# Optimization experiments

Hardware: AMD Instinct MI355X
Metric: run time of the kernel (lower is better)

The kernel has to match this reference:

```python
import jax, jax.numpy as jnp
import numpy as np

NEG_SLOPE = 0.2
EPS = 1e-16


def _gat_layer(x, src, dst, W, a_src, a_dst, b, n_nodes):
    # x: [N, Fin], W: [Fout, Fin]; src/dst: [E'] (self-loops already appended)
    h = x @ W.T                              # [N, Fout]
    alpha_s = h @ a_src                      # [N] per-source score
    alpha_d = h @ a_dst                      # [N] per-dest score
    e = jax.nn.leaky_relu(alpha_s[src] + alpha_d[dst], NEG_SLOPE)  # [E']
    # segment softmax over destination nodes (PyG softmax semantics)
    m = jax.ops.segment_max(e, dst, num_segments=n_nodes)          # [N]
    ex = jnp.exp(e - m[dst])                                       # [E']
    s = jax.ops.segment_sum(ex, dst, num_segments=n_nodes)         # [N]
    alpha = ex / (s[dst] + EPS)                                    # [E']
    out = jax.ops.segment_sum(alpha[:, None] * h[src], dst, num_segments=n_nodes)
    return out + b, alpha


def setup_inputs() -> dict:
    key = jax.random.key(0)
    ks = jax.random.split(key, 14)
    N, E, F_IN, H1, H2, F_OUT = 50000, 800000, 128, 64, 64, 32
    sc = 0.1
    return {
        "x": jax.random.normal(ks[0], (N, F_IN), dtype=jnp.float32),
        "edge_index": jax.random.randint(ks[1], (2, E), 0, N, dtype=jnp.int64),
        "W1": jax.random.normal(ks[2], (H1, F_IN), dtype=jnp.float32) * sc,
        "a_src1": jax.random.normal(ks[3], (H1,), dtype=jnp.float32) * sc,
        "a_dst1": jax.random.normal(ks[4], (H1,), dtype=jnp.float32) * sc,
        "b1": jnp.zeros((H1,), dtype=jnp.float32),
        "W2": jax.random.normal(ks[5], (H2, H1), dtype=jnp.float32) * sc,
        "a_src2": jax.random.normal(ks[6], (H2,), dtype=jnp.float32) * sc,
        "a_dst2": jax.random.normal(ks[7], (H2,), dtype=jnp.float32) * sc,
        "b2": jnp.zeros((H2,), dtype=jnp.float32),
        "W3": jax.random.normal(ks[8], (F_OUT, H2), dtype=jnp.float32) * sc,
        "a_src3": jax.random.normal(ks[9], (F_OUT,), dtype=jnp.float32) * sc,
        "a_dst3": jax.random.normal(ks[10], (F_OUT,), dtype=jnp.float32) * sc,
        "b3": jnp.zeros((F_OUT,), dtype=jnp.float32),
    }


def reference(x, edge_index, W1, a_src1, a_dst1, b1, W2, a_src2, a_dst2, b2, W3, a_src3, a_dst3, b3):
    N = x.shape[0]
    loops = jnp.arange(N, dtype=edge_index.dtype)
    src = jnp.concatenate([edge_index[0], loops])  # add_self_loops=True
    dst = jnp.concatenate([edge_index[1], loops])

    h, alpha1 = _gat_layer(x, src, dst, W1, a_src1, a_dst1, b1, N)
    h = jax.nn.relu(h)
    h, _ = _gat_layer(h, src, dst, W2, a_src2, a_dst2, b2, N)
    h = jax.nn.relu(h)
    out, _ = _gat_layer(h, src, dst, W3, a_src3, a_dst3, b3, N)
    # att_tuple = (edge_index with self loops, attention coefficients of layer 1)
    return (jnp.stack([src, dst]), alpha1, out)
```

## Files before the change

kernel.cpp:

```cpp
#include <hip/hip_runtime.h>
#include <hip/hip_bf16.h>
#include <math.h>

#define NEG_SLOPE 0.2f
#define GAT_EPS 1e-16f

constexpr int NN = 50000;
constexpr int NE = 800000;
constexpr int EP = NE + NN;
constexpr int NB = (NN + 255) / 256;

constexpr int PB  = 128;
constexpr int PT  = 1024;
constexpr int CH  = (EP + PB - 1) / PB;
constexpr int NCH = 4;
constexpr int BPC = PB / NCH;

__device__ inline void edge_sd(const int* __restrict__ ei, int i, int& s, int& d) {
    if (i < NE) { s = ei[i]; d = ei[NE + i]; }
    else        { s = d = i - NE; }
}

__device__ inline float bflo(unsigned int h) { return __uint_as_float(h << 16); }
__device__ inline float bfhi(unsigned int h) { return __uint_as_float(h & 0xffff0000u); }

__global__ __launch_bounds__(PT) void k_p1_hist(const int* __restrict__ ei,
                                                float* __restrict__ out0,
                                                unsigned char* __restrict__ hist,
                                                unsigned char* __restrict__ rank8) {
    __shared__ unsigned int sh[NN / 4];
    int b = blockIdx.x, t = threadIdx.x;
    for (int w = t; w < NN / 4; w += PT) sh[w] = 0u;
    __syncthreads();
    int i0 = b * CH;
    int iend = i0 + CH; if (iend > EP) iend = EP;
    for (int i = i0 + t; i < iend; i += PT) {
        int s, d; edge_sd(ei, i, s, d);
        __builtin_nontemporal_store((float)s, &out0[i]);
        __builtin_nontemporal_store((float)d, &out0[EP + i]);
        int sft = (d & 3) * 8;
        unsigned int old = atomicAdd(&sh[d >> 2], 1u << sft);
        __builtin_nontemporal_store((unsigned char)(old >> sft), &rank8[i]);
    }
    __syncthreads();
    unsigned int* hw = (unsigned int*)(hist + (size_t)b * NN);
    for (int w = t; w < NN / 4; w += PT) hw[w] = sh[w];
}

__global__ __launch_bounds__(256) void k_p2_scan(unsigned char* __restrict__ hist,
                                                 unsigned char* __restrict__ chunksum) {
    int n = blockIdx.x * 256 + threadIdx.x;
    int c = blockIdx.y;
    if (n >= NN) return;
    unsigned int run = 0;
    size_t idx = (size_t)(c * BPC) * NN + n;
    for (int b = 0; b < BPC; ++b, idx += NN) {
        unsigned int v = hist[idx];
        hist[idx] = (unsigned char)run;
        run += v;
    }
    chunksum[n * NCH + c] = (unsigned char)run;
}

__global__ void k_scan1(const unsigned char* __restrict__ chunksum,
                        unsigned char* __restrict__ chunkoff,
                        int* __restrict__ rowptr, int* __restrict__ bsum) {
    __shared__ int sh[256];
    int t = threadIdx.x, i = blockIdx.x * 256 + t;
    int v = 0;
    if (i < NN) {
        unsigned int cs = *(const unsigned int*)&chunksum[i * 4];
        unsigned int c0 = cs & 0xffu, c1 = (cs >> 8) & 0xffu;
        unsigned int c2 = (cs >> 16) & 0xffu, c3 = cs >> 24;
        unsigned int o1 = c0, o2 = c0 + c1, o3 = c0 + c1 + c2;
        *(unsigned int*)&chunkoff[i * 4] = (o1 << 8) | (o2 << 16) | (o3 << 24);
        v = (int)(o3 + c3);
    }
    sh[t] = v; __syncthreads();
    for (int off = 1; off < 256; off <<= 1) {
        int x = (t >= off) ? sh[t - off] : 0;
        __syncthreads();
        sh[t] += x;
        __syncthreads();
    }
    if (i < NN) rowptr[i] = sh[t] - v;
    if (t == 255) bsum[blockIdx.x] = sh[255];
}

__global__ void k_scan2(int* __restrict__ bsum, int* __restrict__ boff) {
    __shared__ int sh[256];
    int t = threadIdx.x;
    int v = (t < NB) ? bsum[t] : 0;
    sh[t] = v; __syncthreads();
    for (int off = 1; off < 256; off <<= 1) {
        int x = (t >= off) ? sh[t - off] : 0;
        __syncthreads();
        sh[t] += x;
        __syncthreads();
    }
    if (t < NB) boff[t] = sh[t] - v;
}

__global__ void k_scan3(int* __restrict__ rowptr, const int* __restrict__ boff) {
    int i = blockIdx.x * blockDim.x + threadIdx.x;
    if (i < NN) rowptr[i] += boff[i >> 8];
    if (i == 0) rowptr[NN] = EP;
}

__global__ __launch_bounds__(PT) void k_fill(const int* __restrict__ ei,
                                             const unsigned char* __restrict__ rank8,
                                             const unsigned char* __restrict__ hist,
                                             const unsigned char* __restrict__ chunkoff,
                                             const int* __restrict__ rowptr,
                                             unsigned short* __restrict__ col) {
    int b = blockIdx.x, t = threadIdx.x;
    int c = b / BPC;
    const unsigned char* __restrict__ hrow = hist + (size_t)b * NN;
    int i0 = b * CH;
    int iend = i0 + CH; if (iend > EP) iend = EP;
    for (int i = i0 + t; i < iend; i += PT) {
        int s, d; edge_sd(ei, i, s, d);
        int pos = rowptr[d] + (int)chunkoff[d * 4 + c] + (int)hrow[d] + (int)rank8[i];
        col[pos] = (unsigned short)s;
    }
}

__global__ void k_alpha_out(const int* __restrict__ ei, const float* __restrict__ as_,
                            const float* __restrict__ ad_, const float* __restrict__ inv,
                            float* __restrict__ out_alpha) {
    int i = blockIdx.x * blockDim.x + threadIdx.x;
    if (i >= EP) return;
    int s, d; edge_sd(ei, i, s, d);
    float v = as_[s] + ad_[d];
    v = v > 0.f ? v : NEG_SLOPE * v;
    __builtin_nontemporal_store(__expf(v) * inv[d], &out_alpha[i]);
}

struct alignas(8) bh4 { __hip_bfloat16 a, b, c, d; };

__device__ inline void fma4(float4& acc, float x, const float4& w) {
    acc.x = fmaf(x, w.x, acc.x);
    acc.y = fmaf(x, w.y, acc.y);
    acc.z = fmaf(x, w.z, acc.z);
    acc.w = fmaf(x, w.w, acc.w);
}

template <int FIN, int FOUT, int NPB>
__global__ __launch_bounds__(256) void k_gemm_t(const float* __restrict__ in,
                                                const float* __restrict__ W,
                                                const float* __restrict__ avs,
                                                const float* __restrict__ avd,
                                                __hip_bfloat16* __restrict__ H,
                                                float* __restrict__ as_,
                                                float* __restrict__ ad_, int n) {
    constexpr int TF = FOUT / 4;
    constexpr int XS = FIN + 4;
    constexpr int WS = FOUT + 4;
    __shared__ float sX[NPB * XS];
    __shared__ float sWt[FIN * WS];
    int tid = threadIdx.x;
    for (int idx = tid; idx < FIN * FOUT; idx += 256) {
        int f = idx % FOUT, k = idx / FOUT;
        sWt[k * WS + f] = W[f * FIN + k];
    }
    int nb = blockIdx.x * NPB;
    for (int idx = tid; idx < NPB * (FIN / 4); idx += 256) {
        int node = idx / (FIN / 4), kq = idx % (FIN / 4);
        int g = nb + node;
        float4 v = make_float4(0.f, 0.f, 0.f, 0.f);
        if (g < n) v = *(const float4*)&in[(size_t)g * FIN + kq * 4];
        *(float4*)&sX[node * XS + kq * 4] = v;
    }
    __syncthreads();

    int fq = tid % TF, ng = tid / TF;
    int n0 = ng * 4;
    float4 acc0 = make_float4(0.f, 0.f, 0.f, 0.f);
    float4 acc1 = acc0, acc2 = acc0, acc3 = acc0;
    for (int k = 0; k < FIN; k += 4) {
        float4 w0 = *(const float4*)&sWt[(k + 0) * WS + fq * 4];
        float4 w1 = *(const float4*)&sWt[(k + 1) * WS + fq * 4];
        float4 w2 = *(const float4*)&sWt[(k + 2) * WS + fq * 4];
        float4 w3 = *(const float4*)&sWt[(k + 3) * WS + fq * 4];
        float4 x0 = *(const float4*)&sX[(n0 + 0) * XS + k];
        float4 x1 = *(const float4*)&sX[(n0 + 1) * XS + k];
        float4 x2 = *(const float4*)&sX[(n0 + 2) * XS + k];
        float4 x3 = *(const float4*)&sX[(n0 + 3) * XS + k];
        fma4(acc0, x0.x, w0); fma4(acc0, x0.y, w1); fma4(acc0, x0.z, w2); fma4(acc0, x0.w, w3);
        fma4(acc1, x1.x, w0); fma4(acc1, x1.y, w1); fma4(acc1, x1.z, w2); fma4(acc1, x1.w, w3);
        fma4(acc2, x2.x, w0); fma4(acc2, x2.y, w1); fma4(acc2, x2.z, w2); fma4(acc2, x2.w, w3);
        fma4(acc3, x3.x, w0); fma4(acc3, x3.y, w1); fma4(acc3, x3.z, w2); fma4(acc3, x3.w, w3);
    }
    float4 accs[4] = {acc0, acc1, acc2, acc3};
    float4 vs4 = *(const float4*)&avs[fq * 4];
    float4 vd4 = *(const float4*)&avd[fq * 4];
#pragma unroll
    for (int j = 0; j < 4; ++j) {
        int g = nb + n0 + j;
        float ps = accs[j].x * vs4.x + accs[j].y * vs4.y + accs[j].z * vs4.z + accs[j].w * vs4.w;
        float pd = accs[j].x * vd4.x + accs[j].y * vd4.y + accs[j].z * vd4.z + accs[j].w * vd4.w;
#pragma unroll
        for (int off = TF / 2; off; off >>= 1) {
            ps += __shfl_down(ps, off, TF);
            pd += __shfl_down(pd, off, TF);
        }
        if (g < n) {
            if (fq == 0) { as_[g] = ps; ad_[g] = pd; }
            bh4 o;
            o.a = __float2bfloat16(accs[j].x);
            o.b = __float2bfloat16(accs[j].y);
            o.c = __float2bfloat16(accs[j].z);
            o.d = __float2bfloat16(accs[j].w);
            *(bh4*)&H[(size_t)g * FOUT + fq * 4] = o;
        }
    }
}

template <int FOUT, bool RELU, bool WRITE_INV>
__global__ __launch_bounds__(256) void k_node_attn(
    const int* __restrict__ rowptr, const unsigned short* __restrict__ col,
    const float* __restrict__ as_, const float* __restrict__ ad_,
    const __hip_bfloat16* __restrict__ H, const float* __restrict__ bias,
    float* __restrict__ outp, float* __restrict__ inv_out) {
    int wid = (blockIdx.x * blockDim.x + threadIdx.x) >> 6;
    int lane = threadIdx.x & 63;
    if (wid >= NN) return;
    int start = rowptr[wid], end = rowptr[wid + 1];
    float adv = ad_[wid];
    const uint2* __restrict__ H4 = (const uint2*)H;

    float sloc = 0.f;
    float ax = 0.f, ay = 0.f, az = 0.f, aw = 0.f;
    for (int c = start; c < end; c += 64) {
        int e = c + lane;
        float p = 0.f;
        int sc = 0;
        if (e < end) {
            sc = (int)col[e];
            float v = as_[sc] + adv;
            v = v > 0.f ? v : NEG_SLOPE * v;
            p = __expf(v);
        }
        sloc += p;
        int cnt = end - c; if (cnt > 64) cnt = 64;
        if (FOUT == 64) {
            int q = lane >> 4, fl = lane & 15;
            int j = 0;
            for (; j + 32 <= cnt; j += 32) {
                float pp[8]; int ss[8]; uint2 hh[8];
#pragma unroll
                for (int k = 0; k < 8; ++k) {
                    int ek = j + 4 * k + q;
                    pp[k] = __shfl(p, ek);
                    ss[k] = __shfl(sc, ek);
                }
#pragma unroll
                for (int k = 0; k < 8; ++k) hh[k] = H4[((size_t)ss[k] << 4) + fl];
#pragma unroll
                for (int k = 0; k < 8; ++k) {
                    ax = fmaf(pp[k], bflo(hh[k].x), ax);
                    ay = fmaf(pp[k], bfhi(hh[k].x), ay);
                    az = fmaf(pp[k], bflo(hh[k].y), az);
                    aw = fmaf(pp[k], bfhi(hh[k].y), aw);
                }
            }
            for (; j + 8 <= cnt; j += 8) {
                int e0 = j + q, e1 = j + 4 + q;
                float p0 = __shfl(p, e0), p1 = __shfl(p, e1);
                int s0 = __shfl(sc, e0), s1 = __shfl(sc, e1);
                uint2 h0 = H4[((size_t)s0 << 4) + fl];
                uint2 h1 = H4[((size_t)s1 << 4) + fl];
                ax = fmaf(p0, bflo(h0.x), ax); ay = fmaf(p0, bfhi(h0.x), ay);
                az = fmaf(p0, bflo(h0.y), az); aw = fmaf(p0, bfhi(h0.y), aw);
                ax = fmaf(p1, bflo(h1.x), ax); ay = fmaf(p1, bfhi(h1.x), ay);
                az = fmaf(p1, bflo(h1.y), az); aw = fmaf(p1, bfhi(h1.y), aw);
            }
            for (; j < cnt; j += 4) {
                int e0 = j + q;
                float p0 = __shfl(p, e0);
                int   s0 = __shfl(sc, e0);
                uint2 h0 = H4[((size_t)s0 << 4) + fl];
                ax = fmaf(p0, bflo(h0.x), ax); ay = fmaf(p0, bfhi(h0.x), ay);
                az = fmaf(p0, bflo(h0.y), az); aw = fmaf(p0, bfhi(h0.y), aw);
            }
        } else {
            int oc = lane >> 3, fl = lane & 7;
            int j = 0;
            for (; j + 32 <= cnt; j += 32) {
                float pp[4]; int ss[4]; uint2 hh[4];
#pragma unroll
                for (int k = 0; k < 4; ++k) {
                    int ek = j + 8 * k + oc;
                    pp[k] = __shfl(p, ek);
                    ss[k] = __shfl(sc, ek);
                }
#pragma unroll
                for (int k = 0; k < 4; ++k) hh[k] = H4[((size_t)ss[k] << 3) + fl];
#pragma unroll
                for (int k = 0; k < 4; ++k) {
                    ax = fmaf(pp[k], bflo(hh[k].x), ax);
                    ay = fmaf(pp[k], bfhi(hh[k].x), ay);
                    az = fmaf(pp[k], bflo(hh[k].y), az);
                    aw = fmaf(pp[k], bfhi(hh[k].y), aw);
                }
            }
            for (; j < cnt; j += 8) {
                int e0 = j + oc;
                float p0 = __shfl(p, e0);
                int   s0 = __shfl(sc, e0);
                uint2 h0 = H4[((size_t)s0 << 3) + fl];
                ax = fmaf(p0, bflo(h0.x), ax); ay = fmaf(p0, bfhi(h0.x), ay);
                az = fmaf(p0, bflo(h0.y), az); aw = fmaf(p0, bfhi(h0.y), aw);
            }
        }
    }
    for (int off = 32; off; off >>= 1) sloc += __shfl_xor(sloc, off);
    float inv = 1.f / (sloc + GAT_EPS);
    if (WRITE_INV && lane == 0) inv_out[wid] = inv;

    if (FOUT == 64) {
        ax += __shfl_xor(ax, 16); ay += __shfl_xor(ay, 16);
        az += __shfl_xor(az, 16); aw += __shfl_xor(aw, 16);
        ax += __shfl_xor(ax, 32); ay += __shfl_xor(ay, 32);
        az += __shfl_xor(az, 32); aw += __shfl_xor(aw, 32);
        if (lane < 16) {
            float4 bb = *(const float4*)&bias[lane * 4];
            float o0 = bb.x + ax * inv;
            float o1 = bb.y + ay * inv;
            float o2 = bb.z + az * inv;
            float o3 = bb.w + aw * inv;
            if (RELU) {
                o0 = fmaxf(o0, 0.f); o1 = fmaxf(o1, 0.f);
                o2 = fmaxf(o2, 0.f); o3 = fmaxf(o3, 0.f);
            }
            *(float4*)&outp[((size_t)wid << 6) + lane * 4] = make_float4(o0, o1, o2, o3);
        }
    } else {
        ax += __shfl_xor(ax, 8);  ay += __shfl_xor(ay, 8);
        az += __shfl_xor(az, 8);  aw += __shfl_xor(aw, 8);
        ax += __shfl_xor(ax, 16); ay += __shfl_xor(ay, 16);
        az += __shfl_xor(az, 16); aw += __shfl_xor(aw, 16);
        ax += __shfl_xor(ax, 32); ay += __shfl_xor(ay, 32);
        az += __shfl_xor(az, 32); aw += __shfl_xor(aw, 32);
        if (lane < 8) {
            float4 bb = *(const float4*)&bias[lane * 4];
            float o0 = bb.x + ax * inv;
            float o1 = bb.y + ay * inv;
            float o2 = bb.z + az * inv;
            float o3 = bb.w + aw * inv;
            if (RELU) {
                o0 = fmaxf(o0, 0.f); o1 = fmaxf(o1, 0.f);
                o2 = fmaxf(o2, 0.f); o3 = fmaxf(o3, 0.f);
            }
            *(float4*)&outp[((size_t)wid << 5) + lane * 4] = make_float4(o0, o1, o2, o3);
        }
    }
}

extern "C" void kernel_launch(void* const* d_in, const int* in_sizes, int n_in,
                              void* d_out, int out_size, void* d_ws, size_t ws_size,
                              hipStream_t stream) {
    const float* x  = (const float*)d_in[0];
    const int*   ei = (const int*)d_in[1];
    const float* W1 = (const float*)d_in[2];
    const float* as1 = (const float*)d_in[3];
    const float* ad1 = (const float*)d_in[4];
    const float* b1 = (const float*)d_in[5];
    const float* W2 = (const float*)d_in[6];
    const float* as2 = (const float*)d_in[7];
    const float* ad2 = (const float*)d_in[8];
    const float* b2 = (const float*)d_in[9];
    const float* W3 = (const float*)d_in[10];
    const float* as3 = (const float*)d_in[11];
    const float* ad3 = (const float*)d_in[12];
    const float* b3 = (const float*)d_in[13];

    float* out = (float*)d_out;
    float* out_edges = out;
    float* out_alpha = out + 2 * EP;
    float* out_final = out + 3 * EP;

    char* w = (char*)d_ws;
    size_t o = 0;
    auto alloc = [&](size_t bytes) { void* p = w + o; o = (o + bytes + 15) & ~15ull; return p; };
    float* as_ = (float*)alloc((size_t)NN * 4);
    float* ad_ = (float*)alloc((size_t)NN * 4);
    float* inv = (float*)alloc((size_t)NN * 4);
    __hip_bfloat16* H = (__hip_bfloat16*)alloc((size_t)NN * 64 * 2);
    int* rowptr = (int*)alloc((size_t)(NN + 1) * 4);
    unsigned char* rank8 = (unsigned char*)alloc((size_t)EP);
    unsigned short* col  = (unsigned short*)alloc((size_t)EP * 2);
    unsigned char* chunksum = (unsigned char*)alloc((size_t)NN * 4);
    unsigned char* chunkoff = (unsigned char*)alloc((size_t)NN * 4);
    int* bsum = (int*)alloc(1024);
    int* boff = (int*)alloc(1024);

    const size_t aggBytes  = (size_t)NN * 64 * 4;
    const size_t histBytes = (size_t)PB * NN;
    float* agg = (ws_size >= o + aggBytes)
        ? (float*)(w + o)
        : (float*)d_in[0];
    unsigned char* hist = (ws_size >= o + aggBytes + histBytes)
        ? (unsigned char*)(w + o + aggBytes)
        : (unsigned char*)out_final;

    k_p1_hist<<<PB, PT, 0, stream>>>(ei, out_edges, hist, rank8);
    k_p2_scan<<<dim3(NB, NCH), 256, 0, stream>>>(hist, chunksum);
    k_scan1<<<NB, 256, 0, stream>>>(chunksum, chunkoff, rowptr, bsum);
    k_scan2<<<1, 256, 0, stream>>>(bsum, boff);
    k_scan3<<<NB, 256, 0, stream>>>(rowptr, boff);
    k_fill<<<PB, PT, 0, stream>>>(ei, rank8, hist, chunkoff, rowptr, col);

    const int nblk = (NN * 64 + 255) / 256;

    k_gemm_t<128, 64, 64><<<(NN + 63) / 64, 256, 0, stream>>>(x, W1, as1, ad1, H, as_, ad_, NN);
    k_node_attn<64, true, true><<<nblk, 256, 0, stream>>>(rowptr, col, as_, ad_, H, b1,
                                                          agg, inv);
    k_alpha_out<<<(EP + 255) / 256, 256, 0, stream>>>(ei, as_, ad_, inv, out_alpha);

    k_gemm_t<64, 64, 64><<<(NN + 63) / 64, 256, 0, stream>>>(agg, W2, as2, ad2, H, as_, ad_, NN);
    k_node_attn<64, true, false><<<nblk, 256, 0, stream>>>(rowptr, col, as_, ad_, H, b2,
                                                           agg, nullptr);

    k_gemm_t<64, 32, 128><<<(NN + 127) / 128, 256, 0, stream>>>(agg, W3, as3, ad3, H, as_, ad_,
                                                                NN);
    k_node_attn<32, false, false><<<nblk, 256, 0, stream>>>(rowptr, col, as_, ad_, H, b3,
                                                            out_final, nullptr);
}
```

Before: 307.9 us.

## Merge scan kernels cooperatively and co-launch independent fill/GEMM and GEMM2/alpha work

The four CSR-building scan kernels become one cooperative kernel that uses grid syncs, with the old launches kept as a fallback if the cooperative launch fails. The col fill runs in the same launch as the layer-1 GEMM, and the layer-2 GEMM shares a launch with the layer-1 alpha output. Double-buffered attention score arrays make the second pairing safe. The goal is fewer launches and less serialization between independent stages, at the cost of fill blocks now using 256 threads instead of 1024 and extra grid-sync overhead.

```diff
diff --git a/kernel.cpp b/kernel.cpp
--- a/kernel.cpp
+++ b/kernel.cpp
@@ -1,6 +1,9 @@
 #include <hip/hip_runtime.h>
 #include <hip/hip_bf16.h>
+#include <hip/hip_cooperative_groups.h>
 #include <math.h>
+
+namespace cg = cooperative_groups;
 
 #define NEG_SLOPE 0.2f
 #define GAT_EPS 1e-16f
@@ -15,6 +18,10 @@
 constexpr int CH  = (EP + PB - 1) / PB;
 constexpr int NCH = 4;
 constexpr int BPC = PB / NCH;
+
+constexpr int GB1 = (NN + 63) / 64;
+constexpr int GB2 = (NN + 63) / 64;
+constexpr int AB  = (EP + 255) / 256;
 
 __device__ inline void edge_sd(const int* __restrict__ ei, int i, int& s, int& d) {
     if (i < NE) { s = ei[i]; d = ei[NE + i]; }
@@ -47,18 +54,80 @@
     for (int w = t; w < NN / 4; w += PT) hw[w] = sh[w];
 }
 
+__global__ __launch_bounds__(256) void k_scans_coop(
+    unsigned char* __restrict__ hist, unsigned char* __restrict__ chunksum,
+    unsigned char* __restrict__ chunkoff, int* __restrict__ rowptr,
+    int* __restrict__ bsum, int* __restrict__ boff) {
+    __shared__ int sh[256];
+    cg::grid_group grid = cg::this_grid();
+    int t = threadIdx.x;
+    int g = blockIdx.x * 256 + t;
+    constexpr int G = NB * 256;
+    for (int u = g; u < NN * NCH; u += G) {
+        int n = u % NN, c = u / NN;
+        int base = (c * BPC) * NN + n;
+        unsigned int v[BPC];
+#pragma unroll
+        for (int b = 0; b < BPC; ++b) v[b] = hist[base + b * NN];
+        unsigned int run = 0;
+#pragma unroll
+        for (int b = 0; b < BPC; ++b) { unsigned int x = v[b]; v[b] = run; run += x; }
+#pragma unroll
+        for (int b = 0; b < BPC; ++b) hist[base + b * NN] = (unsigned char)v[b];
+        chunksum[n * NCH + c] = (unsigned char)run;
+    }
+    grid.sync();
+    {
+        int i = g, vv = 0;
+        if (i < NN) {
+            unsigned int cs = *(const unsigned int*)&chunksum[i * 4];
+            unsigned int c0 = cs & 0xffu, c1 = (cs >> 8) & 0xffu;
+            unsigned int c2 = (cs >> 16) & 0xffu, c3 = cs >> 24;
+            unsigned int o1 = c0, o2 = c0 + c1, o3 = c0 + c1 + c2;
+            *(unsigned int*)&chunkoff[i * 4] = (o1 << 8) | (o2 << 16) | (o3 << 24);
+            vv = (int)(o3 + c3);
+        }
+        sh[t] = vv; __syncthreads();
+        for (int off = 1; off < 256; off <<= 1) {
+            int xx = (t >= off) ? sh[t - off] : 0;
+            __syncthreads();
+            sh[t] += xx;
+            __syncthreads();
+        }
+        if (i < NN) rowptr[i] = sh[t] - vv;
+        if (t == 255) bsum[blockIdx.x] = sh[255];
+    }
+    grid.sync();
+    if (blockIdx.x == 0) {
+        int vv = (t < NB) ? bsum[t] : 0;
+        sh[t] = vv; __syncthreads();
+        for (int off = 1; off < 256; off <<= 1) {
+            int xx = (t >= off) ? sh[t - off] : 0;
+            __syncthreads();
+            sh[t] += xx;
+            __syncthreads();
+        }
+        if (t < NB) boff[t] = sh[t] - vv;
+    }
+    grid.sync();
+    if (g < NN) rowptr[g] += boff[g >> 8];
+    if (g == 0) rowptr[NN] = EP;
+}
+
 __global__ __launch_bounds__(256) void k_p2_scan(unsigned char* __restrict__ hist,
                                                  unsigned char* __restrict__ chunksum) {
     int n = blockIdx.x * 256 + threadIdx.x;
     int c = blockIdx.y;
     if (n >= NN) return;
+    int base = (c * BPC) * NN + n;
+    unsigned int v[BPC];
+#pragma unroll
+    for (int b = 0; b < BPC; ++b) v[b] = hist[base + b * NN];
     unsigned int run = 0;
-    size_t idx = (size_t)(c * BPC) * NN + n;
-    for (int b = 0; b < BPC; ++b, idx += NN) {
-        unsigned int v = hist[idx];
-        hist[idx] = (unsigned char)run;
-        run += v;
-    }
+#pragma unroll
+    for (int b = 0; b < BPC; ++b) { unsigned int x = v[b]; v[b] = run; run += x; }
+#pragma unroll
+    for (int b = 0; b < BPC; ++b) hist[base + b * NN] = (unsigned char)v[b];
     chunksum[n * NCH + c] = (unsigned char)run;
 }
 
@@ -107,35 +176,6 @@
     if (i == 0) rowptr[NN] = EP;
 }
 
-__global__ __launch_bounds__(PT) void k_fill(const int* __restrict__ ei,
-                                             const unsigned char* __restrict__ rank8,
-                                             const unsigned char* __restrict__ hist,
-                                             const unsigned char* __restrict__ chunkoff,
-                                             const int* __restrict__ rowptr,
-                                             unsigned short* __restrict__ col) {
-    int b = blockIdx.x, t = threadIdx.x;
-    int c = b / BPC;
-    const unsigned char* __restrict__ hrow = hist + (size_t)b * NN;
-    int i0 = b * CH;
-    int iend = i0 + CH; if (iend > EP) iend = EP;
-    for (int i = i0 + t; i < iend; i += PT) {
-        int s, d; edge_sd(ei, i, s, d);
-        int pos = rowptr[d] + (int)chunkoff[d * 4 + c] + (int)hrow[d] + (int)rank8[i];
-        col[pos] = (unsigned short)s;
-    }
-}
-
-__global__ void k_alpha_out(const int* __restrict__ ei, const float* __restrict__ as_,
-                            const float* __restrict__ ad_, const float* __restrict__ inv,
-                            float* __restrict__ out_alpha) {
-    int i = blockIdx.x * blockDim.x + threadIdx.x;
-    if (i >= EP) return;
-    int s, d; edge_sd(ei, i, s, d);
-    float v = as_[s] + ad_[d];
-    v = v > 0.f ? v : NEG_SLOPE * v;
-    __builtin_nontemporal_store(__expf(v) * inv[d], &out_alpha[i]);
-}
-
 struct alignas(8) bh4 { __hip_bfloat16 a, b, c, d; };
 
 __device__ inline void fma4(float4& acc, float x, const float4& w) {
@@ -146,24 +186,23 @@
 }
 
 template <int FIN, int FOUT, int NPB>
-__global__ __launch_bounds__(256) void k_gemm_t(const float* __restrict__ in,
-                                                const float* __restrict__ W,
-                                                const float* __restrict__ avs,
-                                                const float* __restrict__ avd,
-                                                __hip_bfloat16* __restrict__ H,
-                                                float* __restrict__ as_,
-                                                float* __restrict__ ad_, int n) {
+__device__ __forceinline__ void gemm_body(float* sX, float* sWt, int bid,
+                                          const float* __restrict__ in,
+                                          const float* __restrict__ W,
+                                          const float* __restrict__ avs,
+                                          const float* __restrict__ avd,
+                                          __hip_bfloat16* __restrict__ H,
+                                          float* __restrict__ as_,
+                                          float* __restrict__ ad_, int n) {
     constexpr int TF = FOUT / 4;
     constexpr int XS = FIN + 4;
     constexpr int WS = FOUT + 4;
-    __shared__ float sX[NPB * XS];
-    __shared__ float sWt[FIN * WS];
     int tid = threadIdx.x;
     for (int idx = tid; idx < FIN * FOUT; idx += 256) {
         int f = idx % FOUT, k = idx / FOUT;
         sWt[k * WS + f] = W[f * FIN + k];
     }
-    int nb = blockIdx.x * NPB;
+    int nb = bid * NPB;
     for (int idx = tid; idx < NPB * (FIN / 4); idx += 256) {
         int node = idx / (FIN / 4), kq = idx % (FIN / 4);
         int g = nb + node;
@@ -216,6 +255,83 @@
     }
 }
 
+__device__ __forceinline__ void fill_body(int b, const int* __restrict__ ei,
+                                          const unsigned char* __restrict__ rank8,
+                                          const unsigned char* __restrict__ hist,
+                                          const unsigned char* __restrict__ chunkoff,
+                                          const int* __restrict__ rowptr,
+                                          unsigned short* __restrict__ col) {
+    int c = b / BPC;
+    const unsigned char* __restrict__ hrow = hist + (size_t)b * NN;
+    int i0 = b * CH;
+    int iend = i0 + CH; if (iend > EP) iend = EP;
+    for (int i = i0 + threadIdx.x; i < iend; i += 256) {
+        int s, d; edge_sd(ei, i, s, d);
+        int pos = rowptr[d] + (int)chunkoff[d * 4 + c] + (int)hrow[d] + (int)rank8[i];
+        col[pos] = (unsigned short)s;
+    }
+}
+
+__global__ __launch_bounds__(256) void k_fill_gemm1(
+    const int* __restrict__ ei, const unsigned char* __restrict__ rank8,
+    const unsigned char* __restrict__ hist, const unsigned char* __restrict__ chunkoff,
+    const int* __restrict__ rowptr, unsigned short* __restrict__ col,
+    const float* __restrict__ x, const float* __restrict__ W1,
+    const float* __restrict__ avs, const float* __restrict__ avd,
+    __hip_bfloat16* __restrict__ H, float* __restrict__ as_, float* __restrict__ ad_) {
+    __shared__ float sX[64 * 132];
+    __shared__ float sWt[128 * 68];
+    int bid = blockIdx.x;
+    if (bid < PB) {
+        fill_body(bid, ei, rank8, hist, chunkoff, rowptr, col);
+    } else {
+        gemm_body<128, 64, 64>(sX, sWt, bid - PB, x, W1, avs, avd, H, as_, ad_, NN);
+    }
+}
+
+__device__ __forceinline__ void alpha_body(int b, const int* __restrict__ ei,
+                                           const float* __restrict__ as_,
+                                           const float* __restrict__ ad_,
+                                           const float* __restrict__ inv,
+                                           float* __restrict__ out_alpha) {
+    int i = b * 256 + threadIdx.x;
+    if (i >= EP) return;
+    int s, d; edge_sd(ei, i, s, d);
+    float v = as_[s] + ad_[d];
+    v = v > 0.f ? v : NEG_SLOPE * v;
+    __builtin_nontemporal_store(__expf(v) * inv[d], &out_alpha[i]);
+}
+
+__global__ __launch_bounds__(256) void k_gemm2_alpha(
+    const float* __restrict__ agg, const float* __restrict__ W2,
+    const float* __restrict__ avs, const float* __restrict__ avd,
+    __hip_bfloat16* __restrict__ H, float* __restrict__ asB, float* __restrict__ adB,
+    const int* __restrict__ ei, const float* __restrict__ asA,
+    const float* __restrict__ adA, const float* __restrict__ inv,
+    float* __restrict__ out_alpha) {
+    __shared__ float sX[64 * 68];
+    __shared__ float sWt[64 * 68];
+    int bid = blockIdx.x;
+    if (bid < GB2) {
+        gemm_body<64, 64, 64>(sX, sWt, bid, agg, W2, avs, avd, H, asB, adB, NN);
+    } else {
+        alpha_body(bid - GB2, ei, asA, adA, inv, out_alpha);
+    }
+}
+
+template <int FIN, int FOUT, int NPB>
+__global__ __launch_bounds__(256) void k_gemm_t(const float* __restrict__ in,
+                                                const float* __restrict__ W,
+                                                const float* __restrict__ avs,
+                                                const float* __restrict__ avd,
+                                                __hip_bfloat16* __restrict__ H,
+                                                float* __restrict__ as_,
+                                                float* __restrict__ ad_, int n) {
+    __shared__ float sX[NPB * (FIN + 4)];
+    __shared__ float sWt[FIN * (FOUT + 4)];
+    gemm_body<FIN, FOUT, NPB>(sX, sWt, blockIdx.x, in, W, avs, avd, H, as_, ad_, n);
+}
+
 template <int FOUT, bool RELU, bool WRITE_INV>
 __global__ __launch_bounds__(256) void k_node_attn(
     const int* __restrict__ rowptr, const unsigned short* __restrict__ col,
@@ -383,8 +499,10 @@
     char* w = (char*)d_ws;
     size_t o = 0;
     auto alloc = [&](size_t bytes) { void* p = w + o; o = (o + bytes + 15) & ~15ull; return p; };
-    float* as_ = (float*)alloc((size_t)NN * 4);
-    float* ad_ = (float*)alloc((size_t)NN * 4);
+    float* asA = (float*)alloc((size_t)NN * 4);
+    float* adA = (float*)alloc((size_t)NN * 4);
+    float* asB = (float*)alloc((size_t)NN * 4);
+    float* adB = (float*)alloc((size_t)NN * 4);
     float* inv = (float*)alloc((size_t)NN * 4);
     __hip_bfloat16* H = (__hip_bfloat16*)alloc((size_t)NN * 64 * 2);
     int* rowptr = (int*)alloc((size_t)(NN + 1) * 4);
@@ -405,25 +523,32 @@
         : (unsigned char*)out_final;
 
     k_p1_hist<<<PB, PT, 0, stream>>>(ei, out_edges, hist, rank8);
-    k_p2_scan<<<dim3(NB, NCH), 256, 0, stream>>>(hist, chunksum);
-    k_scan1<<<NB, 256, 0, stream>>>(chunksum, chunkoff, rowptr, bsum);
-    k_scan2<<<1, 256, 0, stream>>>(bsum, boff);
-    k_scan3<<<NB, 256, 0, stream>>>(rowptr, boff);
-    k_fill<<<PB, PT, 0, stream>>>(ei, rank8, hist, chunkoff, rowptr, col);
+    {
+        void* args[] = {(void*)&hist, (void*)&chunksum, (void*)&chunkoff,
+                        (void*)&rowptr, (void*)&bsum, (void*)&boff};
+        hipError_t e = hipLaunchCooperativeKernel((const void*)k_scans_coop, dim3(NB),
+                                                  dim3(256), args, 0, stream);
+        if (e != hipSuccess) {
+            (void)hipGetLastError();
+            k_p2_scan<<<dim3(NB, NCH), 256, 0, stream>>>(hist, chunksum);
+            k_scan1<<<NB, 256, 0, stream>>>(chunksum, chunkoff, rowptr, bsum);
+            k_scan2<<<1, 256, 0, stream>>>(bsum, boff);
+            k_scan3<<<NB, 256, 0, stream>>>(rowptr, boff);
+        }
+    }
 
     const int nblk = (NN * 64 + 255) / 256;
 
-    k_gemm_t<128, 64, 64><<<(NN + 63) / 64, 256, 0, stream>>>(x, W1, as1, ad1, H, as_, ad_, NN);
-    k_node_attn<64, true, true><<<nblk, 256, 0, stream>>>(rowptr, col, as_, ad_, H, b1,
+    k_fill_gemm1<<<PB + GB1, 256, 0, stream>>>(ei, rank8, hist, chunkoff, rowptr, col,
+                                               x, W1, as1, ad1, H, asA, adA);
+    k_node_attn<64, true, true><<<nblk, 256, 0, stream>>>(rowptr, col, asA, adA, H, b1,
                                                           agg, inv);
-    k_alpha_out<<<(EP + 255) / 256, 256, 0, stream>>>(ei, as_, ad_, inv, out_alpha);
-
-    k_gemm_t<64, 64, 64><<<(NN + 63) / 64, 256, 0, stream>>>(agg, W2, as2, ad2, H, as_, ad_, NN);
-    k_node_attn<64, true, false><<<nblk, 256, 0, stream>>>(rowptr, col, as_, ad_, H, b2,
+    k_gemm2_alpha<<<GB2 + AB, 256, 0, stream>>>(agg, W2, as2, ad2, H, asB, adB,
+                                                ei, asA, adA, inv, out_alpha);
+    k_node_attn<64, true, false><<<nblk, 256, 0, stream>>>(rowptr, col, asB, adB, H, b2,
                                                            agg, nullptr);
-
-    k_gemm_t<64, 32, 128><<<(NN + 127) / 128, 256, 0, stream>>>(agg, W3, as3, ad3, H, as_, ad_,
-                                                                NN);
-    k_node_attn<32, false, false><<<nblk, 256, 0, stream>>>(rowptr, col, as_, ad_, H, b3,
+    k_gemm_t<64, 32, 128><<<(NN + 127) / 128, 256, 0, stream>>>(agg, W3, as3, ad3, H,
+                                                                asA, adA, NN);
+    k_node_attn<32, false, false><<<nblk, 256, 0, stream>>>(rowptr, col, asA, adA, H, b3,
                                                             out_final, nullptr);
 }
```

After: 375.1 us. +21.8%, slower.

## Fuse CSR build scan kernels and flatten fill to one thread per edge

Applied to the files above, without the earlier changes.

Merges the per-chunk histogram scan and the chunk-offset/block scan into one kernel, and merges the block-sum scan with the rowptr offset add by having every block redundantly scan the small block-sum array. This cuts the CSR construction from five launches to three and drops the chunksum and boff buffers. The fill kernel now uses one thread per edge across many small blocks instead of 128 large blocks striding over chunks, which raises parallelism. In exchange, the fused scan kernel has fewer blocks (NB rather than NB×4), so each thread does serial work over all chunks with more registers.

```diff
diff --git a/kernel.cpp b/kernel.cpp
--- a/kernel.cpp
+++ b/kernel.cpp
@@ -47,34 +47,32 @@
     for (int w = t; w < NN / 4; w += PT) hw[w] = sh[w];
 }
 
-__global__ __launch_bounds__(256) void k_p2_scan(unsigned char* __restrict__ hist,
-                                                 unsigned char* __restrict__ chunksum) {
-    int n = blockIdx.x * 256 + threadIdx.x;
-    int c = blockIdx.y;
-    if (n >= NN) return;
-    unsigned int run = 0;
-    size_t idx = (size_t)(c * BPC) * NN + n;
-    for (int b = 0; b < BPC; ++b, idx += NN) {
-        unsigned int v = hist[idx];
-        hist[idx] = (unsigned char)run;
-        run += v;
-    }
-    chunksum[n * NCH + c] = (unsigned char)run;
-}
-
-__global__ void k_scan1(const unsigned char* __restrict__ chunksum,
-                        unsigned char* __restrict__ chunkoff,
-                        int* __restrict__ rowptr, int* __restrict__ bsum) {
+__global__ __launch_bounds__(256) void k_p2s1(unsigned char* __restrict__ hist,
+                                              unsigned char* __restrict__ chunkoff,
+                                              int* __restrict__ rowptr,
+                                              int* __restrict__ bsum) {
     __shared__ int sh[256];
-    int t = threadIdx.x, i = blockIdx.x * 256 + t;
+    int t = threadIdx.x;
+    int n = blockIdx.x * 256 + t;
     int v = 0;
-    if (i < NN) {
-        unsigned int cs = *(const unsigned int*)&chunksum[i * 4];
-        unsigned int c0 = cs & 0xffu, c1 = (cs >> 8) & 0xffu;
-        unsigned int c2 = (cs >> 16) & 0xffu, c3 = cs >> 24;
-        unsigned int o1 = c0, o2 = c0 + c1, o3 = c0 + c1 + c2;
-        *(unsigned int*)&chunkoff[i * 4] = (o1 << 8) | (o2 << 16) | (o3 << 24);
-        v = (int)(o3 + c3);
+    if (n < NN) {
+        unsigned int runs[NCH];
+#pragma unroll
+        for (int c = 0; c < NCH; ++c) {
+            size_t base = (size_t)(c * BPC) * NN + n;
+            unsigned int vv[BPC];
+#pragma unroll
+            for (int b = 0; b < BPC; ++b) vv[b] = hist[base + (size_t)b * NN];
+            unsigned int run = 0;
+#pragma unroll
+            for (int b = 0; b < BPC; ++b) { unsigned int x = vv[b]; vv[b] = run; run += x; }
+#pragma unroll
+            for (int b = 0; b < BPC; ++b) hist[base + (size_t)b * NN] = (unsigned char)vv[b];
+            runs[c] = run;
+        }
+        unsigned int o1 = runs[0], o2 = o1 + runs[1], o3 = o2 + runs[2];
+        *(unsigned int*)&chunkoff[(size_t)n * 4] = (o1 << 8) | (o2 << 16) | (o3 << 24);
+        v = (int)(o3 + runs[3]);
     }
     sh[t] = v; __syncthreads();
     for (int off = 1; off < 256; off <<= 1) {
@@ -83,11 +81,12 @@
         sh[t] += x;
         __syncthreads();
     }
-    if (i < NN) rowptr[i] = sh[t] - v;
+    if (n < NN) rowptr[n] = sh[t] - v;
     if (t == 255) bsum[blockIdx.x] = sh[255];
 }
 
-__global__ void k_scan2(int* __restrict__ bsum, int* __restrict__ boff) {
+__global__ __launch_bounds__(256) void k_s23(int* __restrict__ rowptr,
+                                             const int* __restrict__ bsum) {
     __shared__ int sh[256];
     int t = threadIdx.x;
     int v = (t < NB) ? bsum[t] : 0;
@@ -98,31 +97,27 @@
         sh[t] += x;
         __syncthreads();
     }
-    if (t < NB) boff[t] = sh[t] - v;
-}
-
-__global__ void k_scan3(int* __restrict__ rowptr, const int* __restrict__ boff) {
-    int i = blockIdx.x * blockDim.x + threadIdx.x;
-    if (i < NN) rowptr[i] += boff[i >> 8];
-    if (i == 0) rowptr[NN] = EP;
-}
-
-__global__ __launch_bounds__(PT) void k_fill(const int* __restrict__ ei,
-                                             const unsigned char* __restrict__ rank8,
-                                             const unsigned char* __restrict__ hist,
-                                             const unsigned char* __restrict__ chunkoff,
-                                             const int* __restrict__ rowptr,
-                                             unsigned short* __restrict__ col) {
-    int b = blockIdx.x, t = threadIdx.x;
+    int blk = blockIdx.x;
+    int off = (blk == 0) ? 0 : sh[blk - 1];
+    int n = blk * 256 + t;
+    if (n < NN) rowptr[n] += off;
+    if (n == 0) rowptr[NN] = EP;
+}
+
+__global__ __launch_bounds__(256) void k_fill(const int* __restrict__ ei,
+                                              const unsigned char* __restrict__ rank8,
+                                              const unsigned char* __restrict__ hist,
+                                              const unsigned char* __restrict__ chunkoff,
+                                              const int* __restrict__ rowptr,
+                                              unsigned short* __restrict__ col) {
+    int i = blockIdx.x * 256 + threadIdx.x;
+    if (i >= EP) return;
+    int b = i / CH;
     int c = b / BPC;
-    const unsigned char* __restrict__ hrow = hist + (size_t)b * NN;
-    int i0 = b * CH;
-    int iend = i0 + CH; if (iend > EP) iend = EP;
-    for (int i = i0 + t; i < iend; i += PT) {
-        int s, d; edge_sd(ei, i, s, d);
-        int pos = rowptr[d] + (int)chunkoff[d * 4 + c] + (int)hrow[d] + (int)rank8[i];
-        col[pos] = (unsigned short)s;
-    }
+    int s, d; edge_sd(ei, i, s, d);
+    int pos = rowptr[d] + (int)chunkoff[d * 4 + c] + (int)hist[(size_t)b * NN + d]
+            + (int)rank8[i];
+    col[pos] = (unsigned short)s;
 }
 
 __global__ void k_alpha_out(const int* __restrict__ ei, const float* __restrict__ as_,
@@ -390,10 +385,8 @@
     int* rowptr = (int*)alloc((size_t)(NN + 1) * 4);
     unsigned char* rank8 = (unsigned char*)alloc((size_t)EP);
     unsigned short* col  = (unsigned short*)alloc((size_t)EP * 2);
-    unsigned char* chunksum = (unsigned char*)alloc((size_t)NN * 4);
     unsigned char* chunkoff = (unsigned char*)alloc((size_t)NN * 4);
     int* bsum = (int*)alloc(1024);
-    int* boff = (int*)alloc(1024);
 
     const size_t aggBytes  = (size_t)NN * 64 * 4;
     const size_t histBytes = (size_t)PB * NN;
@@ -405,11 +398,9 @@
         : (unsigned char*)out_final;
 
     k_p1_hist<<<PB, PT, 0, stream>>>(ei, out_edges, hist, rank8);
-    k_p2_scan<<<dim3(NB, NCH), 256, 0, stream>>>(hist, chunksum);
-    k_scan1<<<NB, 256, 0, stream>>>(chunksum, chunkoff, rowptr, bsum);
-    k_scan2<<<1, 256, 0, stream>>>(bsum, boff);
-    k_scan3<<<NB, 256, 0, stream>>>(rowptr, boff);
-    k_fill<<<PB, PT, 0, stream>>>(ei, rank8, hist, chunkoff, rowptr, col);
+    k_p2s1<<<NB, 256, 0, stream>>>(hist, chunkoff, rowptr, bsum);
+    k_s23<<<NB, 256, 0, stream>>>(rowptr, bsum);
+    k_fill<<<(EP + 255) / 256, 256, 0, stream>>>(ei, rank8, hist, chunkoff, rowptr, col);
 
     const int nblk = (NN * 64 + 255) / 256;
 
```

Measured after the change: 292.7 us. -4.9%, faster.
